# Performance work log

Measured on AMD Instinct MI355X. Metric: run time of the kernel, lower is better.

The kernel has to match this reference:

```python
import jax, jax.numpy as jnp
import numpy as np

N = 50000      # num_nodes
E_HALF = 800000  # undirected edge pairs; total directed edges E = 2*E_HALF
D = 4          # sheaf stalk dimension (config.d)
F = 16         # num_features per stalk dim


def setup_inputs() -> dict:
    key = jax.random.key(0)
    k1, k2, k3, k4 = jax.random.split(key, 4)
    src = jax.random.randint(k1, (E_HALF,), 0, N)
    dst = jax.random.randint(k2, (E_HALF,), 0, N)
    # symmetric directed edge set: edge e < E_HALF has reverse e + E_HALF
    edge_index = jnp.stack([jnp.concatenate([src, dst]),
                            jnp.concatenate([dst, src])])  # [2, E]
    rev_idx = jnp.concatenate([jnp.arange(E_HALF) + E_HALF,
                               jnp.arange(E_HALF)])        # [E]
    x = jax.random.normal(k3, (N, D, F), dtype=jnp.float32)
    restriction_maps = jax.random.normal(k4, (2 * E_HALF, D, D), dtype=jnp.float32)
    return {"x": x, "restriction_maps": restriction_maps,
            "edge_index": edge_index, "rev_idx": rev_idx}


def reference(x, restriction_maps, edge_index, rev_idx):
    # Dirichlet energy, normalize=False (D_u^{-1/2} = I):
    # loss = sum_e || F_{v->u} x[v] - F_{u->v} x[u] ||_F^2
    src, tgt = edge_index[0], edge_index[1]
    Fuv = restriction_maps               # [E, d, d]  maps[e]
    Fvu = restriction_maps[rev_idx]      # [E, d, d]  maps[reverse(e)]
    term1 = jnp.einsum('eij,ejf->eif', Fvu, x[tgt])  # [E, d, F]
    term2 = jnp.einsum('eij,ejf->eif', Fuv, x[src])  # [E, d, F]
    diff = term1 - term2
    return jnp.sum(diff * diff)
```

## Files before the change

### kernel.cpp

```cpp
#include <hip/hip_runtime.h>


typedef float f4 __attribute__((ext_vector_type(4)));
typedef unsigned int u32;

#define EPB 128

__device__ __forceinline__ f4 ld4(const float* p) {
    return *reinterpret_cast<const f4*>(p);
}

__device__ __forceinline__ f4 unpk(u32 w0, u32 w1) {
    f4 r;
    r.x = __builtin_bit_cast(float, w0 << 16);
    r.y = __builtin_bit_cast(float, w0 & 0xFFFF0000u);
    r.z = __builtin_bit_cast(float, w1 << 16);
    r.w = __builtin_bit_cast(float, w1 & 0xFFFF0000u);
    return r;
}

__global__ __launch_bounds__(256) void conv_kernel(
    const float* __restrict__ x, unsigned short* __restrict__ xb, int total )
{
    const int idx = blockIdx.x * blockDim.x + threadIdx.x;
    if (idx >= total) return;
    const int node = idx >> 2;
    const int q    = idx & 3;
    const float* p = x + (size_t)node * 64 + q * 4;
    unsigned short outv[16];
    #pragma unroll
    for (int j = 0; j < 4; ++j) {
        const f4 v = ld4(p + j * 16);
        #pragma unroll
        for (int c = 0; c < 4; ++c) {
            const u32 b = __builtin_bit_cast(u32, v[c]);
            const u32 r = b + 0x7FFFu + ((b >> 16) & 1u);
            outv[j * 4 + c] = (unsigned short)(r >> 16);
        }
    }
    unsigned short* dst = xb + (size_t)node * 64 + q * 16;
    *reinterpret_cast<uint4*>(dst)     = *reinterpret_cast<const uint4*>(outv);
    *reinterpret_cast<uint4*>(dst + 8) = *reinterpret_cast<const uint4*>(outv + 8);
}

#define MSTRIDE 20

__global__ __launch_bounds__(256) void sheaf_energy_lds(
    const unsigned short* __restrict__ xb,
    const float* __restrict__ maps,
    const int*   __restrict__ edge_index,
    float* __restrict__ partials,
    int eHalf, int E)
{
    __shared__ float m2l[EPB * MSTRIDE];
    __shared__ float m1l[EPB * MSTRIDE];
    __shared__ float wave_sums[4];

    const int t    = threadIdx.x;
    const int base = blockIdx.x * EPB;

    const float* m2g = maps + (size_t)base * 16;
    const float* m1g = maps + ((size_t)base + (size_t)eHalf) * 16;
    #pragma unroll
    for (int rep = 0; rep < 2; ++rep) {
        const int f_   = t * 4 + rep * 1024;
        const int slot = f_ >> 4;
        const int off  = f_ & 15;
        *reinterpret_cast<f4*>(&m2l[slot * MSTRIDE + off]) = ld4(m2g + f_);
        *reinterpret_cast<f4*>(&m1l[slot * MSTRIDE + off]) = ld4(m1g + f_);
    }
    __syncthreads();

    float ssum = 0.0f;

    #pragma unroll
    for (int p = 0; p < 2; ++p) {
        const int slot = p * 64 + (t >> 2);
        const int q    = t & 3;
        const int e    = base + slot;

        const int sn = edge_index[e];
        const int tn = edge_index[E + e];

        const unsigned short* xtp = xb + (size_t)tn * 64 + q * 16;
        const unsigned short* xsp = xb + (size_t)sn * 64 + q * 16;
        const uint4 ta = *reinterpret_cast<const uint4*>(xtp);
        const uint4 tb = *reinterpret_cast<const uint4*>(xtp + 8);
        const uint4 sa = *reinterpret_cast<const uint4*>(xsp);
        const uint4 sb = *reinterpret_cast<const uint4*>(xsp + 8);

        const f4 xt0 = unpk(ta.x, ta.y);
        const f4 xt1 = unpk(ta.z, ta.w);
        const f4 xt2 = unpk(tb.x, tb.y);
        const f4 xt3 = unpk(tb.z, tb.w);
        const f4 xs0 = unpk(sa.x, sa.y);
        const f4 xs1 = unpk(sa.z, sa.w);
        const f4 xs2 = unpk(sb.x, sb.y);
        const f4 xs3 = unpk(sb.z, sb.w);

        const float* m1b = &m1l[slot * MSTRIDE];
        const float* m2b = &m2l[slot * MSTRIDE];

        #pragma unroll
        for (int i = 0; i < 4; ++i) {
            const f4 m1 = *reinterpret_cast<const f4*>(m1b + i * 4);
            const f4 m2 = *reinterpret_cast<const f4*>(m2b + i * 4);
            f4 d = {0.f, 0.f, 0.f, 0.f};
            d += m1.x * xt0;
            d += m1.y * xt1;
            d += m1.z * xt2;
            d += m1.w * xt3;
            d -= m2.x * xs0;
            d -= m2.y * xs1;
            d -= m2.z * xs2;
            d -= m2.w * xs3;
            ssum += d.x * d.x + d.y * d.y + d.z * d.z + d.w * d.w;
        }
    }

    #pragma unroll
    for (int off = 32; off > 0; off >>= 1)
        ssum += __shfl_down(ssum, off, 64);

    const int lane = t & 63;
    const int wid  = t >> 6;
    if (lane == 0) wave_sums[wid] = ssum;
    __syncthreads();
    if (t == 0)
        partials[blockIdx.x] = wave_sums[0] + wave_sums[1]
                             + wave_sums[2] + wave_sums[3];
}

__global__ __launch_bounds__(256) void sheaf_energy_bf16(
    const unsigned short* __restrict__ xb, const float* __restrict__ maps,
    const int* __restrict__ edge_index, float* __restrict__ partials,
    int eHalf, int E, int nGroups)
{
    const int tid = blockIdx.x * blockDim.x + threadIdx.x;
    const int gid = tid >> 4;
    const int i   = (threadIdx.x >> 2) & 3;
    const int q   = threadIdx.x & 3;
    float ssum = 0.0f;
    #pragma unroll 2
    for (int k = 0; k < 8; ++k) {
        const int e = gid + k * nGroups;
        if (e >= eHalf) break;
        const int s = edge_index[e];
        const int t = edge_index[E + e];
        const f4 m1 = ld4(maps + (size_t)(e + eHalf) * 16 + i * 4);
        const f4 m2 = ld4(maps + (size_t)e * 16 + i * 4);
        const unsigned short* xtp = xb + (size_t)t * 64 + q * 16;
        const unsigned short* xsp = xb + (size_t)s * 64 + q * 16;
        const uint4 ta = *reinterpret_cast<const uint4*>(xtp);
        const uint4 tb = *reinterpret_cast<const uint4*>(xtp + 8);
        const uint4 sa = *reinterpret_cast<const uint4*>(xsp);
        const uint4 sb = *reinterpret_cast<const uint4*>(xsp + 8);
        const f4 xt0 = unpk(ta.x, ta.y), xt1 = unpk(ta.z, ta.w);
        const f4 xt2 = unpk(tb.x, tb.y), xt3 = unpk(tb.z, tb.w);
        const f4 xs0 = unpk(sa.x, sa.y), xs1 = unpk(sa.z, sa.w);
        const f4 xs2 = unpk(sb.x, sb.y), xs3 = unpk(sb.z, sb.w);
        f4 d = {0.f, 0.f, 0.f, 0.f};
        d += m1.x * xt0;  d += m1.y * xt1;  d += m1.z * xt2;  d += m1.w * xt3;
        d -= m2.x * xs0;  d -= m2.y * xs1;  d -= m2.z * xs2;  d -= m2.w * xs3;
        ssum += d.x * d.x + d.y * d.y + d.z * d.z + d.w * d.w;
    }
    #pragma unroll
    for (int off = 32; off > 0; off >>= 1)
        ssum += __shfl_down(ssum, off, 64);
    __shared__ float wave_sums[4];
    const int lane = threadIdx.x & 63;
    const int wid  = threadIdx.x >> 6;
    if (lane == 0) wave_sums[wid] = ssum;
    __syncthreads();
    if (threadIdx.x == 0)
        partials[blockIdx.x] = wave_sums[0] + wave_sums[1]
                             + wave_sums[2] + wave_sums[3];
}

__global__ __launch_bounds__(1024) void reduce_kernel(
    const float* __restrict__ partials, int n, float* __restrict__ out)
{
    float a0 = 0.f, a1 = 0.f, a2 = 0.f, a3 = 0.f;
    int idx = threadIdx.x;
    for (; idx + 3 * 1024 < n; idx += 4 * 1024) {
        a0 += partials[idx];
        a1 += partials[idx + 1024];
        a2 += partials[idx + 2048];
        a3 += partials[idx + 3072];
    }
    for (; idx < n; idx += 1024) a0 += partials[idx];
    float s = (a0 + a1) + (a2 + a3);
    #pragma unroll
    for (int off = 32; off > 0; off >>= 1)
        s += __shfl_down(s, off, 64);
    __shared__ float wsum[16];
    const int lane = threadIdx.x & 63;
    const int wid  = threadIdx.x >> 6;
    if (lane == 0) wsum[wid] = s;
    __syncthreads();
    if (threadIdx.x == 0) {
        float tot = 0.0f;
        #pragma unroll
        for (int k = 0; k < 16; ++k) tot += wsum[k];
        out[0] = 2.0f * tot;
    }
}

extern "C" void kernel_launch(void* const* d_in, const int* in_sizes, int n_in,
                              void* d_out, int out_size, void* d_ws, size_t ws_size,
                              hipStream_t stream) {
    const float* x          = (const float*)d_in[0];
    const float* maps       = (const float*)d_in[1];
    const int*   edge_index = (const int*)d_in[2];
    float* out = (float*)d_out;

    const int E     = in_sizes[3];
    const int eHalf = E / 2;
    const int N     = in_sizes[0] / 64;

    const int block = 256;
    const int grid  = (eHalf + EPB - 1) / EPB;

    const size_t xbBytes = (size_t)N * 64 * sizeof(unsigned short);
    const size_t need    = xbBytes + (size_t)grid * sizeof(float);

    if (ws_size >= need && (eHalf % EPB) == 0) {
        unsigned short* xb = (unsigned short*)d_ws;
        float* partials    = (float*)((char*)d_ws + xbBytes);

        const int total    = N * 4;
        const int convGrid = (total + block - 1) / block;
        conv_kernel<<<convGrid, block, 0, stream>>>(x, xb, total);
        sheaf_energy_lds<<<grid, block, 0, stream>>>(xb, maps, edge_index,
                                                     partials, eHalf, E);
        reduce_kernel<<<1, 1024, 0, stream>>>(partials, grid, out);
    } else if (ws_size >= need) {
        unsigned short* xb = (unsigned short*)d_ws;
        float* partials    = (float*)((char*)d_ws + xbBytes);
        const int nGroups  = grid * 16;
        const int total    = N * 4;
        const int convGrid = (total + block - 1) / block;
        conv_kernel<<<convGrid, block, 0, stream>>>(x, xb, total);
        sheaf_energy_bf16<<<grid, block, 0, stream>>>(xb, maps, edge_index,
                                                      partials, eHalf, E, nGroups);
        reduce_kernel<<<1, 1024, 0, stream>>>(partials, grid, out);
    } else {
        float* partials = (float*)d_ws;
        const int nGroups = grid * 16;
        sheaf_energy_bf16<<<grid, block, 0, stream>>>((const unsigned short*)x,
                                                      maps, edge_index,
                                                      partials, eHalf, E, nGroups);
        reduce_kernel<<<1, 1024, 0, stream>>>(partials, grid, out);
    }
}
```

Measured before the change: 48.47 us.

## Stream restriction maps into LDS directly and batch all edge gathers up front

Replaces the LDS-staged energy kernel with one that doubles edges per block. Restriction maps are copied straight from global memory into LDS with global_load_lds, using a swizzled layout that each wave reads back itself, so no block barrier is needed. All edge indices and all bf16 node gathers for four edges per thread are issued before any compute. Staged s_waitcnt vmcnt waits then let the math for each edge start while later gathers are still in flight. The goal is more outstanding memory requests per wave and fewer barriers, at the cost of more registers and fragile hand-written asm wait counts.

```diff
diff --git a/kernel.cpp b/kernel.cpp
--- a/kernel.cpp
+++ b/kernel.cpp
@@ -3,8 +3,21 @@
 
 typedef float f4 __attribute__((ext_vector_type(4)));
 typedef unsigned int u32;
-
-#define EPB 128
+typedef u32 u32x4 __attribute__((ext_vector_type(4)));
+
+#define EPB 256
+
+#define GLD4U(dst, ptr) \
+    asm volatile("global_load_dwordx4 %0, %1, off" : "=v"(dst) : "v"(ptr))
+#define GLDI(dst, ptr) \
+    asm volatile("global_load_dword %0, %1, off" : "=v"(dst) : "v"(ptr))
+#define SBAR() __builtin_amdgcn_sched_barrier(0)
+
+__device__ __forceinline__ void gload_lds16(const float* g, float* l) {
+    __builtin_amdgcn_global_load_lds(
+        (const __attribute__((address_space(1))) void*)g,
+        (__attribute__((address_space(3))) void*)l, 16, 0, 0);
+}
 
 __device__ __forceinline__ f4 ld4(const float* p) {
     return *reinterpret_cast<const f4*>(p);
@@ -43,68 +56,82 @@
     *reinterpret_cast<uint4*>(dst + 8) = *reinterpret_cast<const uint4*>(outv + 8);
 }
 
-#define MSTRIDE 20
-
-__global__ __launch_bounds__(256) void sheaf_energy_lds(
+__global__ __launch_bounds__(256) void sheaf_energy_dma(
     const unsigned short* __restrict__ xb,
     const float* __restrict__ maps,
     const int*   __restrict__ edge_index,
     float* __restrict__ partials,
     int eHalf, int E)
 {
-    __shared__ float m2l[EPB * MSTRIDE];
-    __shared__ float m1l[EPB * MSTRIDE];
+    __shared__ float m2l[EPB * 16];
+    __shared__ float m1l[EPB * 16];
     __shared__ float wave_sums[4];
 
     const int t    = threadIdx.x;
+    const int lane = t & 63;
+    const int w    = t >> 6;
     const int base = blockIdx.x * EPB;
 
     const float* m2g = maps + (size_t)base * 16;
-    const float* m1g = maps + ((size_t)base + (size_t)eHalf) * 16;
-    #pragma unroll
-    for (int rep = 0; rep < 2; ++rep) {
-        const int f_   = t * 4 + rep * 1024;
-        const int slot = f_ >> 4;
-        const int off  = f_ & 15;
-        *reinterpret_cast<f4*>(&m2l[slot * MSTRIDE + off]) = ld4(m2g + f_);
-        *reinterpret_cast<f4*>(&m1l[slot * MSTRIDE + off]) = ld4(m1g + f_);
-    }
-    __syncthreads();
+    const float* m1g = m2g + (size_t)eHalf * 16;
+    const int lsw = (lane & 15) * 16 + (lane >> 4) * 4;
+    #pragma unroll
+    for (int p = 0; p < 4; ++p) {
+        const int r = p * 4 + w;
+        gload_lds16(m2g + r * 256 + lsw, &m2l[r * 256]);
+        gload_lds16(m1g + r * 256 + lsw, &m1l[r * 256]);
+    }
+
+    int sv[4], tv[4];
+    #pragma unroll
+    for (int p = 0; p < 4; ++p) {
+        const int e = base + p * 64 + (t >> 2);
+        GLDI(sv[p], edge_index + e);
+        GLDI(tv[p], edge_index + E + e);
+    }
+    asm volatile("s_waitcnt vmcnt(0)" ::: "memory");
+    SBAR();
+
+    const int q = t & 3;
+    u32x4 xta[4], xtb[4], xsa[4], xsb[4];
+    #pragma unroll
+    for (int p = 0; p < 4; ++p) {
+        const unsigned short* xtp = xb + (size_t)tv[p] * 64 + q * 16;
+        const unsigned short* xsp = xb + (size_t)sv[p] * 64 + q * 16;
+        GLD4U(xta[p], xtp);
+        GLD4U(xtb[p], xtp + 8);
+        GLD4U(xsa[p], xsp);
+        GLD4U(xsb[p], xsp + 8);
+    }
 
     float ssum = 0.0f;
-
-    #pragma unroll
-    for (int p = 0; p < 2; ++p) {
-        const int slot = p * 64 + (t >> 2);
-        const int q    = t & 3;
-        const int e    = base + slot;
-
-        const int sn = edge_index[e];
-        const int tn = edge_index[E + e];
-
-        const unsigned short* xtp = xb + (size_t)tn * 64 + q * 16;
-        const unsigned short* xsp = xb + (size_t)sn * 64 + q * 16;
-        const uint4 ta = *reinterpret_cast<const uint4*>(xtp);
-        const uint4 tb = *reinterpret_cast<const uint4*>(xtp + 8);
-        const uint4 sa = *reinterpret_cast<const uint4*>(xsp);
-        const uint4 sb = *reinterpret_cast<const uint4*>(xsp + 8);
-
-        const f4 xt0 = unpk(ta.x, ta.y);
-        const f4 xt1 = unpk(ta.z, ta.w);
-        const f4 xt2 = unpk(tb.x, tb.y);
-        const f4 xt3 = unpk(tb.z, tb.w);
-        const f4 xs0 = unpk(sa.x, sa.y);
-        const f4 xs1 = unpk(sa.z, sa.w);
-        const f4 xs2 = unpk(sb.x, sb.y);
-        const f4 xs3 = unpk(sb.z, sb.w);
-
-        const float* m1b = &m1l[slot * MSTRIDE];
-        const float* m2b = &m2l[slot * MSTRIDE];
+    const int sl = (t >> 2) & 15;
+
+    #pragma unroll
+    for (int p = 0; p < 4; ++p) {
+        if      (p == 0) { asm volatile("s_waitcnt vmcnt(12)" ::: "memory"); }
+        else if (p == 1) { asm volatile("s_waitcnt vmcnt(8)"  ::: "memory"); }
+        else if (p == 2) { asm volatile("s_waitcnt vmcnt(4)"  ::: "memory"); }
+        else             { asm volatile("s_waitcnt vmcnt(0)"  ::: "memory"); }
+        SBAR();
+
+        const f4 xt0 = unpk(xta[p].x, xta[p].y);
+        const f4 xt1 = unpk(xta[p].z, xta[p].w);
+        const f4 xt2 = unpk(xtb[p].x, xtb[p].y);
+        const f4 xt3 = unpk(xtb[p].z, xtb[p].w);
+        const f4 xs0 = unpk(xsa[p].x, xsa[p].y);
+        const f4 xs1 = unpk(xsa[p].z, xsa[p].w);
+        const f4 xs2 = unpk(xsb[p].x, xsb[p].y);
+        const f4 xs3 = unpk(xsb[p].z, xsb[p].w);
+
+        const int r = p * 4 + w;
+        const float* m1b = &m1l[r * 256 + sl * 4];
+        const float* m2b = &m2l[r * 256 + sl * 4];
 
         #pragma unroll
         for (int i = 0; i < 4; ++i) {
-            const f4 m1 = *reinterpret_cast<const f4*>(m1b + i * 4);
-            const f4 m2 = *reinterpret_cast<const f4*>(m2b + i * 4);
+            const f4 m1 = ld4(m1b + i * 64);
+            const f4 m2 = ld4(m2b + i * 64);
             f4 d = {0.f, 0.f, 0.f, 0.f};
             d += m1.x * xt0;
             d += m1.y * xt1;
@@ -122,9 +149,7 @@
     for (int off = 32; off > 0; off >>= 1)
         ssum += __shfl_down(ssum, off, 64);
 
-    const int lane = t & 63;
-    const int wid  = t >> 6;
-    if (lane == 0) wave_sums[wid] = ssum;
+    if (lane == 0) wave_sums[w] = ssum;
     __syncthreads();
     if (t == 0)
         partials[blockIdx.x] = wave_sums[0] + wave_sums[1]
@@ -231,7 +256,7 @@
         const int total    = N * 4;
         const int convGrid = (total + block - 1) / block;
         conv_kernel<<<convGrid, block, 0, stream>>>(x, xb, total);
-        sheaf_energy_lds<<<grid, block, 0, stream>>>(xb, maps, edge_index,
+        sheaf_energy_dma<<<grid, block, 0, stream>>>(xb, maps, edge_index,
                                                      partials, eHalf, E);
         reduce_kernel<<<1, 1024, 0, stream>>>(partials, grid, out);
     } else if (ws_size >= need) {
```

New measurement: 50.28 us. +3.7%, slower.
